# Performance work log

Hardware: AMD Instinct MI355X
Metric: run time of the kernel (lower is better)

The kernel has to match this reference:

```python
import jax, jax.numpy as jnp
import numpy as np

HIDDEN_SIZE = 2048
NUM_Q_HEADS = 16
NUM_KV_HEADS = 4
HEAD_DIM = 128
EPS = 1e-6
B, T = 1, 4096


def rms_norm(x, w):
    xf = x.astype(jnp.float32)
    n = xf * jax.lax.rsqrt(jnp.mean(xf * xf, axis=-1, keepdims=True) + EPS)
    return (n * w.astype(jnp.float32)).astype(x.dtype)


def rotate_half(x):
    x1, x2 = jnp.split(x, 2, axis=-1)
    return jnp.concatenate([-x2, x1], axis=-1)


def apply_rope(x, cos, sin):
    # x: [B, H, T, D]; cos/sin: [B, T, D]
    return x * cos[:, None, :, :] + rotate_half(x) * sin[:, None, :, :]


def setup_inputs() -> dict:
    key = jax.random.key(0)
    ks = jax.random.split(key, 6)
    s = 0.02
    x = jax.random.normal(ks[0], (B, T, HIDDEN_SIZE), dtype=jnp.float32)
    position_ids = jnp.arange(T, dtype=jnp.int64 if jax.config.jax_enable_x64 else jnp.int32)[None, :].repeat(B, axis=0)
    inv_freq = (1.0 / (10000.0 ** (np.arange(0, HEAD_DIM, 2, dtype=np.float32) / HEAD_DIM))).astype(np.float32)
    inv_freq = jnp.asarray(inv_freq)
    Wq = jax.random.normal(ks[1], (HIDDEN_SIZE, NUM_Q_HEADS * HEAD_DIM * 2), dtype=jnp.float32) * s
    Wk = jax.random.normal(ks[2], (HIDDEN_SIZE, NUM_KV_HEADS * HEAD_DIM), dtype=jnp.float32) * s
    Wv = jax.random.normal(ks[3], (HIDDEN_SIZE, NUM_KV_HEADS * HEAD_DIM), dtype=jnp.float32) * s
    Wo = jax.random.normal(ks[4], (NUM_Q_HEADS * HEAD_DIM, HIDDEN_SIZE), dtype=jnp.float32) * s
    q_norm_w = jnp.ones((HEAD_DIM,), dtype=jnp.float32)
    k_norm_w = jnp.ones((HEAD_DIM,), dtype=jnp.float32)
    return {"x": x, "position_ids": position_ids, "inv_freq": inv_freq,
            "Wq": Wq, "Wk": Wk, "Wv": Wv, "Wo": Wo,
            "q_norm_w": q_norm_w, "k_norm_w": k_norm_w}


def reference(x, position_ids, inv_freq, Wq, Wk, Wv, Wo, q_norm_w, k_norm_w):
    Bb, Tt, _ = x.shape
    dtype = x.dtype
    qg = (x @ Wq).reshape(Bb, Tt, NUM_Q_HEADS, HEAD_DIM * 2)
    q, gate = qg[..., :HEAD_DIM], qg[..., HEAD_DIM:]
    gate = gate.reshape(Bb, Tt, NUM_Q_HEADS * HEAD_DIM)
    k = (x @ Wk).reshape(Bb, Tt, NUM_KV_HEADS, HEAD_DIM)
    v = (x @ Wv).reshape(Bb, Tt, NUM_KV_HEADS, HEAD_DIM)
    q = rms_norm(q, q_norm_w)
    k = rms_norm(k, k_norm_w)
    q = q.transpose(0, 2, 1, 3)  # [B, Hq, T, D]
    k = k.transpose(0, 2, 1, 3)  # [B, Hkv, T, D]
    v = v.transpose(0, 2, 1, 3)
    # RoPE angles: [B, T, D/2] -> concat -> [B, T, D]
    freqs = position_ids.astype(jnp.float32)[:, :, None] * inv_freq[None, None, :]
    emb = jnp.concatenate([freqs, freqs], axis=-1)
    cos, sin = jnp.cos(emb).astype(dtype), jnp.sin(emb).astype(dtype)
    q = apply_rope(q, cos, sin)
    k = apply_rope(k, cos, sin)
    groups = NUM_Q_HEADS // NUM_KV_HEADS
    k = jnp.repeat(k, groups, axis=1)  # [B, Hq, T, D]
    v = jnp.repeat(v, groups, axis=1)
    scale = HEAD_DIM ** -0.5
    attn = jnp.einsum('bhqd,bhkd->bhqk', q, k) * scale
    causal = jnp.tril(jnp.ones((Tt, Tt), dtype=bool))
    attn = jnp.where(causal[None, None, :, :], attn, jnp.array(-jnp.inf, dtype=attn.dtype))
    attn = jax.nn.softmax(attn.astype(jnp.float32), axis=-1).astype(dtype)
    out = jnp.einsum('bhqk,bhkd->bhqd', attn, v)
    out = out.transpose(0, 2, 1, 3).reshape(Bb, Tt, NUM_Q_HEADS * HEAD_DIM)
    out = out * jax.nn.sigmoid(gate)
    return out @ Wo
```

## Files before the change

### kernel.cpp

```cpp
#include <hip/hip_runtime.h>
#include <hip/hip_bf16.h>

#define T_SEQ 4096
#define HID 2048
#define NQH 16
#define NKVH 4
#define HD 128
#define KVW (NKVH * HD)
#define KVSTRIDE 1024
#define QGW (NQH * HD * 2)

typedef __attribute__((ext_vector_type(8))) short short8;
typedef __attribute__((ext_vector_type(4))) float f32x4;
typedef __attribute__((ext_vector_type(16))) float f32x16;
typedef __hip_bfloat16 bf16;

__device__ inline float bf2f(bf16 v) { return __bfloat162float(v); }
__device__ inline bf16 f2bf(float v) { return __float2bfloat16(v); }

__device__ inline void storeC(float* p, float v) { *p = v; }
__device__ inline void storeC(bf16* p, float v) { *p = f2bf(v); }

__device__ inline void gload16(const void* g, void* l) {
    __builtin_amdgcn_global_load_lds(
        (const __attribute__((address_space(1))) void*)g,
        (__attribute__((address_space(3))) void*)l, 16, 0, 0);
}

__device__ inline unsigned pack2(float a, float b) {
    union { bf16 h[2]; unsigned u; } x;
    x.h[0] = f2bf(a); x.h[1] = f2bf(b);
    return x.u;
}
union U8 { unsigned u[4]; short8 s; };

__global__ void rope_tables(const int* __restrict__ pos, const float* __restrict__ inv_freq,
                            float* __restrict__ cosT, float* __restrict__ sinT) {
    int id = blockIdx.x * 256 + threadIdx.x;
    int t = id >> 6, i = id & 63;
    float f = (float)pos[t] * inv_freq[i];
    cosT[id] = cosf(f);
    sinT[id] = sinf(f);
}

__global__ void cvt_bf16(const float* __restrict__ in, bf16* __restrict__ out, int n) {
    int id = (blockIdx.x * 256 + threadIdx.x) * 4;
    if (id >= n) return;
    float4 v = *(const float4*)(in + id);
    bf16 tmp[4] = {f2bf(v.x), f2bf(v.y), f2bf(v.z), f2bf(v.w)};
    *(uint2*)(out + id) = *(uint2*)tmp;
}

__global__ void cvt_transpose(const float* __restrict__ in, bf16* __restrict__ out, int R, int C) {
    __shared__ float tile[32][33];
    int tx = threadIdx.x, ty = threadIdx.y;
    int r0 = blockIdx.y * 32, c0 = blockIdx.x * 32;
#pragma unroll
    for (int k = 0; k < 4; ++k)
        tile[ty + 8 * k][tx] = in[(long)(r0 + ty + 8 * k) * C + c0 + tx];
    __syncthreads();
#pragma unroll
    for (int k = 0; k < 4; ++k)
        out[(long)(c0 + ty + 8 * k) * R + r0 + tx] = f2bf(tile[tx][ty + 8 * k]);
}

__global__ void transpose_v(const bf16* __restrict__ kvb, bf16* __restrict__ vT) {
    __shared__ bf16 tile[32][33];
    int tx = threadIdx.x, ty = threadIdx.y;
    int d0 = blockIdx.x * 32, t0 = blockIdx.y * 32;
#pragma unroll
    for (int k = 0; k < 4; ++k)
        tile[ty + 8 * k][tx] = kvb[(long)(t0 + ty + 8 * k) * KVSTRIDE + KVW + d0 + tx];
    __syncthreads();
#pragma unroll
    for (int k = 0; k < 4; ++k)
        vT[(long)(d0 + ty + 8 * k) * T_SEQ + t0 + tx] = tile[tx][ty + 8 * k];
}

template <typename OutT>
__global__ __launch_bounds__(256) void gemm_bt(const bf16* __restrict__ A,
                                               const bf16* __restrict__ Bt,
                                               OutT* __restrict__ C, int M, int N, int K) {
    __shared__ __align__(16) bf16 As[128 * 32];
    __shared__ __align__(16) bf16 Bs[128 * 32];
    const int tid = threadIdx.x, lane = tid & 63, wv = tid >> 6;
    const int nwg = gridDim.x * gridDim.y;
    const int orig = blockIdx.y * gridDim.x + blockIdx.x;
    const int wg = (orig & 7) * (nwg >> 3) + (orig >> 3);
    const int bm = (wg / gridDim.x) * 128, bn = (wg % gridDim.x) * 128;
    const int wm = (wv >> 1) * 64, wn = (wv & 1) * 64;
    const int lr = lane & 15, lg = lane >> 4;
    f32x4 acc[4][4] = {};
    const int srow = tid >> 2, skg = (tid & 3) * 8;
    const bf16* aP = A + (long)(bm + srow) * K + skg;
    const bf16* bP = Bt + (long)(bn + srow) * K + skg;
    bf16* asBase = As + wv * 512;
    bf16* bsBase = Bs + wv * 512;
    for (int kt = 0; kt < K; kt += 32) {
        __syncthreads();
        gload16(aP + kt, asBase);
        gload16(aP + (long)64 * K + kt, asBase + 2048);
        gload16(bP + kt, bsBase);
        gload16(bP + (long)64 * K + kt, bsBase + 2048);
        __syncthreads();
        short8 af[4], bfv[4];
#pragma unroll
        for (int m = 0; m < 4; ++m)
            af[m] = *(const short8*)(As + (wm + m * 16 + lr) * 32 + lg * 8);
#pragma unroll
        for (int n = 0; n < 4; ++n)
            bfv[n] = *(const short8*)(Bs + (wn + n * 16 + lr) * 32 + lg * 8);
#pragma unroll
        for (int m = 0; m < 4; ++m)
#pragma unroll
            for (int n = 0; n < 4; ++n)
                acc[m][n] = __builtin_amdgcn_mfma_f32_16x16x32_bf16(af[m], bfv[n], acc[m][n], 0, 0, 0);
    }
#pragma unroll
    for (int m = 0; m < 4; ++m)
#pragma unroll
        for (int n = 0; n < 4; ++n)
#pragma unroll
            for (int j = 0; j < 4; ++j) {
                int r = bm + wm + m * 16 + lg * 4 + j;
                int c = bn + wn + n * 16 + lr;
                storeC(&C[(long)r * N + c], acc[m][n][j]);
            }
}

#define STAGEA256(T, hh)                                                                     \
    {                                                                                        \
        const int b_ = (T) & 1;                                                              \
        gload16(aSrc + (long)((hh) * 128) * K + (long)(T) * 64, &As[b_][(hh) * 8192 + wv * 512]); \
        gload16(aSrc + (long)((hh) * 128 + 64) * K + (long)(T) * 64,                         \
                &As[b_][(hh) * 8192 + 4096 + wv * 512]);                                     \
    }
#define STAGEB256(T, hh)                                                                     \
    {                                                                                        \
        const int b_ = (T) & 1;                                                              \
        gload16(bSrc + (long)((hh) * 128) * K + (long)(T) * 64, &Bs[b_][(hh) * 8192 + wv * 512]); \
        gload16(bSrc + (long)((hh) * 128 + 64) * K + (long)(T) * 64,                         \
                &Bs[b_][(hh) * 8192 + 4096 + wv * 512]);                                     \
    }

template <typename OutT>
__global__ __launch_bounds__(512, 2) void gemm256(const bf16* __restrict__ A,
                                                  const bf16* __restrict__ Bt,
                                                  OutT* __restrict__ C, int M, int N, int K) {
    __shared__ __align__(16) bf16 As[2][256 * 64];
    __shared__ __align__(16) bf16 Bs[2][256 * 64];
    const int tid = threadIdx.x, lane = tid & 63, wv = tid >> 6;
    const int wr = wv >> 2, wc = wv & 3;
    const int lr = lane & 15, lg = lane >> 4;
    const int bm = blockIdx.y * 256, bn = blockIdx.x * 256;
    const int nt = K >> 6;

    const int srow = tid >> 3, sslot = tid & 7;
    const int slotLog = sslot ^ (srow & 7);
    const bf16* aSrc = A + (long)(bm + srow) * K + slotLog * 8;
    const bf16* bSrc = Bt + (long)(bn + srow) * K + slotLog * 8;

    int slotE[2];
#pragma unroll
    for (int ks = 0; ks < 2; ++ks) slotE[ks] = ((ks * 4 + lg) ^ (lr & 7)) * 8;

    f32x4 acc[8][4] = {};

    STAGEB256(0, 0); STAGEB256(0, 1);
    STAGEA256(0, 0); STAGEA256(0, 1);
    STAGEB256(1, 0); STAGEB256(1, 1);
    asm volatile("s_waitcnt vmcnt(4)" ::: "memory");
    __builtin_amdgcn_s_barrier();

    for (int t = 0; t < nt; ++t) {
        const int cur = t & 1;
        const bf16* Acur = As[cur];
        const bf16* Bcur = Bs[cur];
        short8 bfr[8];
#pragma unroll
        for (int q = 0; q < 4; ++q) {
            if (q == 0) {
#pragma unroll
                for (int fn = 0; fn < 4; ++fn)
#pragma unroll
                    for (int ks = 0; ks < 2; ++ks)
                        bfr[fn * 2 + ks] =
                            *(const short8*)(Bcur + (wc * 64 + fn * 16 + lr) * 64 + slotE[ks]);
            }
            short8 afr[4];
#pragma unroll
            for (int f2 = 0; f2 < 2; ++f2)
#pragma unroll
                for (int ks = 0; ks < 2; ++ks)
                    afr[f2 * 2 + ks] =
                        *(const short8*)(Acur + (wr * 128 + (q * 2 + f2) * 16 + lr) * 64 + slotE[ks]);
            if (q == 0) { if (t + 1 < nt) STAGEA256(t + 1, 0); }
            else if (q == 1) { if (t + 1 < nt) STAGEA256(t + 1, 1); }
            else if (q == 2) { if (t + 2 < nt) STAGEB256(t + 2, 0); }
            else { if (t + 2 < nt) STAGEB256(t + 2, 1); }
            __builtin_amdgcn_s_barrier();
            __builtin_amdgcn_s_setprio(1);
#pragma unroll
            for (int f2 = 0; f2 < 2; ++f2)
#pragma unroll
                for (int fn = 0; fn < 4; ++fn)
#pragma unroll
                    for (int ks = 0; ks < 2; ++ks)
                        acc[q * 2 + f2][fn] = __builtin_amdgcn_mfma_f32_16x16x32_bf16(
                            afr[f2 * 2 + ks], bfr[fn * 2 + ks], acc[q * 2 + f2][fn], 0, 0, 0);
            __builtin_amdgcn_s_setprio(0);
            if (q == 3) asm volatile("s_waitcnt vmcnt(4)" ::: "memory");
            __builtin_amdgcn_s_barrier();
        }
    }

#pragma unroll
    for (int fm = 0; fm < 8; ++fm)
#pragma unroll
        for (int fn = 0; fn < 4; ++fn)
#pragma unroll
            for (int j = 0; j < 4; ++j) {
                int r = bm + wr * 128 + fm * 16 + lg * 4 + j;
                int c = bn + wc * 64 + fn * 16 + lr;
                storeC(&C[(long)r * N + c], acc[fm][fn][j]);
            }
}

__global__ __launch_bounds__(256) void norm_rope(bf16* __restrict__ buf, int rowStride,
                                                 int headStride, int hshift,
                                                 const float* __restrict__ w,
                                                 const float* __restrict__ cosT,
                                                 const float* __restrict__ sinT,
                                                 float outScale) {
    int row = blockIdx.x * 4 + (threadIdx.x >> 6);
    int lane = threadIdx.x & 63;
    int t = row >> hshift, h = row & ((1 << hshift) - 1);
    bf16* p = buf + (long)t * rowStride + h * headStride;
    float x1 = bf2f(p[lane]), x2 = bf2f(p[lane + 64]);
    float ss = x1 * x1 + x2 * x2;
    ss += __shfl_xor(ss, 1);
    ss += __shfl_xor(ss, 2);
    ss += __shfl_xor(ss, 4);
    ss += __shfl_xor(ss, 8);
    ss += __shfl_xor(ss, 16);
    ss += __shfl_xor(ss, 32);
    float r = rsqrtf(ss * (1.0f / 128.0f) + 1e-6f);
    float c = cosT[t * 64 + lane], s = sinT[t * 64 + lane];
    float n1 = x1 * r * w[lane], n2 = x2 * r * w[lane + 64];
    p[lane] = f2bf((n1 * c - n2 * s) * outScale);
    p[lane + 64] = f2bf((n2 * c + n1 * s) * outScale);
}

__global__ __launch_bounds__(256, 2) void attn9(const bf16* __restrict__ qg,
                                                const bf16* __restrict__ kvb,
                                                const bf16* __restrict__ vT,
                                                bf16* __restrict__ aout) {
    __shared__ __align__(16) bf16 Ks[2][64 * 128];
    __shared__ __align__(16) bf16 Vs[2][128 * 64];
    const int tid = threadIdx.x, lane = tid & 63, wv = tid >> 6;
    const int q32 = lane & 31, g = lane >> 5;
    const int bid = blockIdx.x;
    const int xcd = bid & 7, slot = bid >> 3;
    const int h = 2 * xcd + (slot & 1);
    const int chunk = 31 - (slot >> 1);
    const int hk = h >> 2;
    const int q0w = chunk * 128 + wv * 32;
    const int nkt = 2 * chunk + 2;
    const int qr = q0w + q32;

    short8 bq[8];
    {
        const bf16* qp = qg + (long)(q0w + q32) * QGW + h * (HD * 2) + g * 8;
#pragma unroll
        for (int kk = 0; kk < 8; ++kk) bq[kk] = *(const short8*)(qp + kk * 16);
    }

    f32x16 acc[4] = {};
    f32x16 accL = {};
    float m2 = -1e30f;
    const short8 vONE = {16256, 16256, 16256, 16256, 16256, 16256, 16256, 16256};

    const bf16* kS[4];
    const bf16* vS[4];
    int kOff[4], vOff[4];
#pragma unroll
    for (int i = 0; i < 4; ++i) {
        const int kc = wv * 4 + i;
        const int krow = kc * 4 + (lane >> 4);
        const int kcolB = ((lane & 15) * 16) ^ ((krow & 15) << 4);
        kS[i] = kvb + (long)krow * KVSTRIDE + hk * HD + (kcolB >> 1);
        kOff[i] = kc * 512;
        const int vc = wv * 4 + i;
        const int vrow = vc * 8 + (lane >> 3);
        const int vcolB = ((lane & 7) * 16) ^ ((vrow & 7) << 4);
        vS[i] = vT + (long)(hk * HD + vrow) * T_SEQ + (vcolB >> 1);
        vOff[i] = vc * 512;
    }

#pragma unroll
    for (int i = 0; i < 4; ++i) gload16(kS[i], &Ks[0][kOff[i]]);
#pragma unroll
    for (int i = 0; i < 4; ++i) gload16(vS[i], &Vs[0][vOff[i]]);
    __syncthreads();

    const int kSlotB = (g * 16) ^ ((q32 & 15) << 4);
    const int vSlotB = (g * 16) ^ ((q32 & 7) << 4);

    for (int kt = 0; kt < nkt; ++kt) {
        const int cur = kt & 1;
        if (kt + 1 < nkt) {
            const long koff = (long)(kt + 1) * 64;
#pragma unroll
            for (int i = 0; i < 4; ++i) gload16(kS[i] + koff * KVSTRIDE, &Ks[cur ^ 1][kOff[i]]);
#pragma unroll
            for (int i = 0; i < 4; ++i) gload16(vS[i] + koff, &Vs[cur ^ 1][vOff[i]]);
        }
        const int key00 = kt * 64;
        if (key00 <= q0w + 31) {
            const bf16* KsB = Ks[cur];
            const bf16* VsB = Vs[cur];
            f32x16 s0 = {}, s1 = {};
#pragma unroll
            for (int kk = 0; kk < 8; ++kk) {
                const int ko = q32 * 128 + (((kk * 32) ^ kSlotB) >> 1);
                short8 ka0 = *(const short8*)(KsB + ko);
                short8 ka1 = *(const short8*)(KsB + ko + 4096);
                s0 = __builtin_amdgcn_mfma_f32_32x32x16_bf16(ka0, bq[kk], s0, 0, 0, 0);
                s1 = __builtin_amdgcn_mfma_f32_32x32x16_bf16(ka1, bq[kk], s1, 0, 0, 0);
            }
            if (key00 + 63 > q0w) {
#pragma unroll
                for (int r = 0; r < 16; ++r) {
                    const int krow = (r & 3) + 8 * (r >> 2) + 4 * g;
                    if (key00 + krow > qr) s0[r] = -1e30f;
                    if (key00 + 32 + krow > qr) s1[r] = -1e30f;
                }
            }
            float t8[8];
#pragma unroll
            for (int i = 0; i < 8; ++i)
                t8[i] = fmaxf(fmaxf(s0[i], s0[i + 8]), fmaxf(s1[i], s1[i + 8]));
            float mx = fmaxf(fmaxf(fmaxf(t8[0], t8[1]), fmaxf(t8[2], t8[3])),
                             fmaxf(fmaxf(t8[4], t8[5]), fmaxf(t8[6], t8[7])));
            mx = fmaxf(mx, __shfl_xor(mx, 32));
            float mn = m2, e = 1.f;
            bool need = false;
            if (mx > m2 + 8.f) { mn = mx; e = exp2f(m2 - mx); need = true; }
            m2 = mn;
#pragma unroll
            for (int r = 0; r < 16; ++r) {
                s0[r] = exp2f(s0[r] - mn);
                s1[r] = exp2f(s1[r] - mn);
            }
            if (__any(need)) {
#pragma unroll
                for (int r = 0; r < 16; ++r) {
                    const int krow = (r & 3) + 8 * (r >> 2) + 4 * g;
                    float er = __shfl(e, krow);
#pragma unroll
                    for (int n = 0; n < 4; ++n) acc[n][r] *= er;
                    accL[r] *= er;
                }
            }
            short8 pa[4];
#pragma unroll
            for (int half = 0; half < 2; ++half) {
                const f32x16& p = half ? s1 : s0;
                unsigned lo0 = pack2(p[0], p[1]),   lo1 = pack2(p[2], p[3]);
                unsigned hi0 = pack2(p[4], p[5]),   hi1 = pack2(p[6], p[7]);
                unsigned lo2 = pack2(p[8], p[9]),   lo3 = pack2(p[10], p[11]);
                unsigned hi2 = pack2(p[12], p[13]), hi3 = pack2(p[14], p[15]);
                unsigned sw0 = __shfl_xor(g ? lo0 : hi0, 32);
                unsigned sw1 = __shfl_xor(g ? lo1 : hi1, 32);
                unsigned sw2 = __shfl_xor(g ? lo2 : hi2, 32);
                unsigned sw3 = __shfl_xor(g ? lo3 : hi3, 32);
                U8 a0, a1;
                a0.u[0] = g ? sw0 : lo0;  a0.u[1] = g ? sw1 : lo1;
                a0.u[2] = g ? hi0 : sw0;  a0.u[3] = g ? hi1 : sw1;
                a1.u[0] = g ? sw2 : lo2;  a1.u[1] = g ? sw3 : lo3;
                a1.u[2] = g ? hi2 : sw2;  a1.u[3] = g ? hi3 : sw3;
                pa[half * 2] = a0.s;
                pa[half * 2 + 1] = a1.s;
            }
#pragma unroll
            for (int ks = 0; ks < 4; ++ks) {
                const int vo = q32 * 64 + (((ks * 32) ^ vSlotB) >> 1);
#pragma unroll
                for (int n = 0; n < 4; ++n) {
                    short8 vb = *(const short8*)(VsB + vo + n * 2048);
                    acc[n] = __builtin_amdgcn_mfma_f32_32x32x16_bf16(pa[ks], vb, acc[n], 0, 0, 0);
                }
                accL = __builtin_amdgcn_mfma_f32_32x32x16_bf16(pa[ks], vONE, accL, 0, 0, 0);
            }
        }
        __syncthreads();
    }

#pragma unroll
    for (int r = 0; r < 16; ++r) {
        const int krow = (r & 3) + 8 * (r >> 2) + 4 * g;
        const float linv = 1.0f / accL[r];
        const long t = q0w + krow;
        const bf16* gp = qg + t * QGW + h * (HD * 2) + HD + q32;
        bf16* op = aout + t * (NQH * HD) + h * HD + q32;
#pragma unroll
        for (int n = 0; n < 4; ++n) {
            float gv = bf2f(gp[n * 32]);
            float o = acc[n][r] * linv * (1.f / (1.f + __expf(-gv)));
            op[n * 32] = f2bf(o);
        }
    }
}

extern "C" void kernel_launch(void* const* d_in, const int* in_sizes, int n_in,
                              void* d_out, int out_size, void* d_ws, size_t ws_size,
                              hipStream_t stream) {
    const float* x = (const float*)d_in[0];
    const int* pos = (const int*)d_in[1];
    const float* inv_freq = (const float*)d_in[2];
    const float* Wq = (const float*)d_in[3];
    const float* Wk = (const float*)d_in[4];
    const float* Wv = (const float*)d_in[5];
    const float* Wo = (const float*)d_in[6];
    const float* qw = (const float*)d_in[7];
    const float* kw = (const float*)d_in[8];
    float* out = (float*)d_out;

    char* ws = (char*)d_ws;
    float* cosT = (float*)ws;               ws += (long)T_SEQ * 64 * 4;
    float* sinT = (float*)ws;               ws += (long)T_SEQ * 64 * 4;
    bf16* bx = (bf16*)ws;                   ws += (long)T_SEQ * HID * 2;
    bf16* bWq = (bf16*)ws;                  ws += (long)QGW * HID * 2;
    bf16* bKV = (bf16*)ws;                  ws += (long)KVSTRIDE * HID * 2;
    bf16* bWo = (bf16*)ws;                  ws += (long)HID * HID * 2;
    bf16* qg = (bf16*)ws;                   ws += (long)T_SEQ * QGW * 2;
    bf16* kvb = (bf16*)ws;                  ws += (long)T_SEQ * KVSTRIDE * 2;
    bf16* aout = (bf16*)ws;                 ws += (long)T_SEQ * (NQH * HD) * 2;
    bf16* vT = (bf16*)bWq;

    rope_tables<<<T_SEQ * 64 / 256, 256, 0, stream>>>(pos, inv_freq, cosT, sinT);
    cvt_bf16<<<(T_SEQ * HID / 4 + 255) / 256, 256, 0, stream>>>(x, bx, T_SEQ * HID);
    cvt_transpose<<<dim3(QGW / 32, HID / 32), dim3(32, 8), 0, stream>>>(Wq, bWq, HID, QGW);
    cvt_transpose<<<dim3(KVW / 32, HID / 32), dim3(32, 8), 0, stream>>>(Wk, bKV, HID, KVW);
    cvt_transpose<<<dim3(KVW / 32, HID / 32), dim3(32, 8), 0, stream>>>(Wv, bKV + (long)KVW * HID, HID, KVW);
    cvt_transpose<<<dim3(HID / 32, HID / 32), dim3(32, 8), 0, stream>>>(Wo, bWo, HID, HID);

    gemm256<bf16><<<dim3(QGW / 256, T_SEQ / 256), 512, 0, stream>>>(bx, bWq, qg, T_SEQ, QGW, HID);
    gemm_bt<bf16><<<dim3(KVSTRIDE / 128, T_SEQ / 128), 256, 0, stream>>>(bx, bKV, kvb, T_SEQ, KVSTRIDE, HID);

    transpose_v<<<dim3(KVW / 32, T_SEQ / 32), dim3(32, 8), 0, stream>>>(kvb, vT);
    norm_rope<<<(T_SEQ * NQH) / 4, 256, 0, stream>>>(qg, QGW, HD * 2, 4, qw, cosT, sinT,
                                                     0.08838834764831845f * 1.4426950408889634f);
    norm_rope<<<(T_SEQ * NKVH) / 4, 256, 0, stream>>>(kvb, KVSTRIDE, HD, 2, kw, cosT, sinT, 1.0f);

    attn9<<<dim3(512), 256, 0, stream>>>(qg, kvb, vT, aout);

    gemm256<float><<<dim3(HID / 256, T_SEQ / 256), 512, 0, stream>>>(aout, bWo, out, T_SEQ, HID, NQH * HD);
}
```

Measured before the change: 364.6 us.

## Single-buffer K tile in attention for higher occupancy; narrow output GEMM tile

The attention kernel drops the double-buffered K tile in shared memory, adds a barrier after QK^T, and then prefetches the next K tile, raising launch bounds to 3 blocks per CU. The output projection GEMM becomes templated on tile width and uses BN=128, which doubles the block count (256 instead of 128) to fill more CUs. The cost is an extra sync per key tile and less K prefetch overlap in attention, plus lower per-block reuse in the GEMM.

```diff
diff --git a/kernel.cpp b/kernel.cpp
--- a/kernel.cpp
+++ b/kernel.cpp
@@ -128,31 +128,17 @@
             }
 }
 
-#define STAGEA256(T, hh)                                                                     \
-    {                                                                                        \
-        const int b_ = (T) & 1;                                                              \
-        gload16(aSrc + (long)((hh) * 128) * K + (long)(T) * 64, &As[b_][(hh) * 8192 + wv * 512]); \
-        gload16(aSrc + (long)((hh) * 128 + 64) * K + (long)(T) * 64,                         \
-                &As[b_][(hh) * 8192 + 4096 + wv * 512]);                                     \
-    }
-#define STAGEB256(T, hh)                                                                     \
-    {                                                                                        \
-        const int b_ = (T) & 1;                                                              \
-        gload16(bSrc + (long)((hh) * 128) * K + (long)(T) * 64, &Bs[b_][(hh) * 8192 + wv * 512]); \
-        gload16(bSrc + (long)((hh) * 128 + 64) * K + (long)(T) * 64,                         \
-                &Bs[b_][(hh) * 8192 + 4096 + wv * 512]);                                     \
-    }
-
-template <typename OutT>
+template <int BN, typename OutT>
 __global__ __launch_bounds__(512, 2) void gemm256(const bf16* __restrict__ A,
                                                   const bf16* __restrict__ Bt,
                                                   OutT* __restrict__ C, int M, int N, int K) {
+    constexpr int FN = BN / 64;
     __shared__ __align__(16) bf16 As[2][256 * 64];
-    __shared__ __align__(16) bf16 Bs[2][256 * 64];
+    __shared__ __align__(16) bf16 Bs[2][BN * 64];
     const int tid = threadIdx.x, lane = tid & 63, wv = tid >> 6;
     const int wr = wv >> 2, wc = wv & 3;
     const int lr = lane & 15, lg = lane >> 4;
-    const int bm = blockIdx.y * 256, bn = blockIdx.x * 256;
+    const int bm = blockIdx.y * 256, bn = blockIdx.x * BN;
     const int nt = K >> 6;
 
     const int srow = tid >> 3, sslot = tid & 7;
@@ -160,32 +146,46 @@
     const bf16* aSrc = A + (long)(bm + srow) * K + slotLog * 8;
     const bf16* bSrc = Bt + (long)(bn + srow) * K + slotLog * 8;
 
+    auto stageA = [&](int T, int hh) {
+        const int b_ = T & 1;
+        gload16(aSrc + (long)(hh * 128) * K + (long)T * 64, &As[b_][hh * 8192 + wv * 512]);
+        gload16(aSrc + (long)(hh * 128 + 64) * K + (long)T * 64, &As[b_][hh * 8192 + 4096 + wv * 512]);
+    };
+    auto stageB = [&](int T, int hh) {
+        const int b_ = T & 1;
+        gload16(bSrc + (long)(hh * 128) * K + (long)T * 64, &Bs[b_][hh * 8192 + wv * 512]);
+        gload16(bSrc + (long)(hh * 128 + 64) * K + (long)T * 64, &Bs[b_][hh * 8192 + 4096 + wv * 512]);
+    };
+
     int slotE[2];
 #pragma unroll
     for (int ks = 0; ks < 2; ++ks) slotE[ks] = ((ks * 4 + lg) ^ (lr & 7)) * 8;
 
-    f32x4 acc[8][4] = {};
-
-    STAGEB256(0, 0); STAGEB256(0, 1);
-    STAGEA256(0, 0); STAGEA256(0, 1);
-    STAGEB256(1, 0); STAGEB256(1, 1);
-    asm volatile("s_waitcnt vmcnt(4)" ::: "memory");
+    f32x4 acc[8][FN] = {};
+
+    stageB(0, 0);
+    if constexpr (BN == 256) stageB(0, 1);
+    stageA(0, 0); stageA(0, 1);
+    stageB(1, 0);
+    if constexpr (BN == 256) stageB(1, 1);
+    if constexpr (BN == 256) asm volatile("s_waitcnt vmcnt(4)" ::: "memory");
+    else                     asm volatile("s_waitcnt vmcnt(2)" ::: "memory");
     __builtin_amdgcn_s_barrier();
 
     for (int t = 0; t < nt; ++t) {
         const int cur = t & 1;
         const bf16* Acur = As[cur];
         const bf16* Bcur = Bs[cur];
-        short8 bfr[8];
+        short8 bfr[FN * 2];
 #pragma unroll
         for (int q = 0; q < 4; ++q) {
             if (q == 0) {
 #pragma unroll
-                for (int fn = 0; fn < 4; ++fn)
+                for (int fn = 0; fn < FN; ++fn)
 #pragma unroll
                     for (int ks = 0; ks < 2; ++ks)
                         bfr[fn * 2 + ks] =
-                            *(const short8*)(Bcur + (wc * 64 + fn * 16 + lr) * 64 + slotE[ks]);
+                            *(const short8*)(Bcur + (wc * (BN / 4) + fn * 16 + lr) * 64 + slotE[ks]);
             }
             short8 afr[4];
 #pragma unroll
@@ -194,22 +194,25 @@
                 for (int ks = 0; ks < 2; ++ks)
                     afr[f2 * 2 + ks] =
                         *(const short8*)(Acur + (wr * 128 + (q * 2 + f2) * 16 + lr) * 64 + slotE[ks]);
-            if (q == 0) { if (t + 1 < nt) STAGEA256(t + 1, 0); }
-            else if (q == 1) { if (t + 1 < nt) STAGEA256(t + 1, 1); }
-            else if (q == 2) { if (t + 2 < nt) STAGEB256(t + 2, 0); }
-            else { if (t + 2 < nt) STAGEB256(t + 2, 1); }
+            if (q == 0) { if (t + 1 < nt) stageA(t + 1, 0); }
+            else if (q == 1) { if (t + 1 < nt) stageA(t + 1, 1); }
+            else if (q == 2) { if (t + 2 < nt) stageB(t + 2, 0); }
+            else { if (BN == 256 && t + 2 < nt) stageB(t + 2, 1); }
             __builtin_amdgcn_s_barrier();
             __builtin_amdgcn_s_setprio(1);
 #pragma unroll
             for (int f2 = 0; f2 < 2; ++f2)
 #pragma unroll
-                for (int fn = 0; fn < 4; ++fn)
+                for (int fn = 0; fn < FN; ++fn)
 #pragma unroll
                     for (int ks = 0; ks < 2; ++ks)
                         acc[q * 2 + f2][fn] = __builtin_amdgcn_mfma_f32_16x16x32_bf16(
                             afr[f2 * 2 + ks], bfr[fn * 2 + ks], acc[q * 2 + f2][fn], 0, 0, 0);
             __builtin_amdgcn_s_setprio(0);
-            if (q == 3) asm volatile("s_waitcnt vmcnt(4)" ::: "memory");
+            if (q == 3) {
+                if constexpr (BN == 256) asm volatile("s_waitcnt vmcnt(4)" ::: "memory");
+                else                     asm volatile("s_waitcnt vmcnt(2)" ::: "memory");
+            }
             __builtin_amdgcn_s_barrier();
         }
     }
@@ -217,11 +220,11 @@
 #pragma unroll
     for (int fm = 0; fm < 8; ++fm)
 #pragma unroll
-        for (int fn = 0; fn < 4; ++fn)
+        for (int fn = 0; fn < FN; ++fn)
 #pragma unroll
             for (int j = 0; j < 4; ++j) {
                 int r = bm + wr * 128 + fm * 16 + lg * 4 + j;
-                int c = bn + wc * 64 + fn * 16 + lr;
+                int c = bn + wc * (BN / 4) + fn * 16 + lr;
                 storeC(&C[(long)r * N + c], acc[fm][fn][j]);
             }
 }
@@ -251,11 +254,11 @@
     p[lane + 64] = f2bf((n2 * c + n1 * s) * outScale);
 }
 
-__global__ __launch_bounds__(256, 2) void attn9(const bf16* __restrict__ qg,
-                                                const bf16* __restrict__ kvb,
-                                                const bf16* __restrict__ vT,
-                                                bf16* __restrict__ aout) {
-    __shared__ __align__(16) bf16 Ks[2][64 * 128];
+__global__ __launch_bounds__(256, 3) void attn10(const bf16* __restrict__ qg,
+                                                 const bf16* __restrict__ kvb,
+                                                 const bf16* __restrict__ vT,
+                                                 bf16* __restrict__ aout) {
+    __shared__ __align__(16) bf16 Ks[64 * 128];
     __shared__ __align__(16) bf16 Vs[2][128 * 64];
     const int tid = threadIdx.x, lane = tid & 63, wv = tid >> 6;
     const int q32 = lane & 31, g = lane >> 5;
@@ -298,7 +301,7 @@
     }
 
 #pragma unroll
-    for (int i = 0; i < 4; ++i) gload16(kS[i], &Ks[0][kOff[i]]);
+    for (int i = 0; i < 4; ++i) gload16(kS[i], &Ks[kOff[i]]);
 #pragma unroll
     for (int i = 0; i < 4; ++i) gload16(vS[i], &Vs[0][vOff[i]]);
     __syncthreads();
@@ -308,26 +311,31 @@
 
     for (int kt = 0; kt < nkt; ++kt) {
         const int cur = kt & 1;
+        const int key00 = kt * 64;
+        const bool compute = (key00 <= q0w + 31);
         if (kt + 1 < nkt) {
             const long koff = (long)(kt + 1) * 64;
 #pragma unroll
-            for (int i = 0; i < 4; ++i) gload16(kS[i] + koff * KVSTRIDE, &Ks[cur ^ 1][kOff[i]]);
-#pragma unroll
             for (int i = 0; i < 4; ++i) gload16(vS[i] + koff, &Vs[cur ^ 1][vOff[i]]);
         }
-        const int key00 = kt * 64;
-        if (key00 <= q0w + 31) {
-            const bf16* KsB = Ks[cur];
-            const bf16* VsB = Vs[cur];
-            f32x16 s0 = {}, s1 = {};
+        f32x16 s0 = {}, s1 = {};
+        if (compute) {
 #pragma unroll
             for (int kk = 0; kk < 8; ++kk) {
                 const int ko = q32 * 128 + (((kk * 32) ^ kSlotB) >> 1);
-                short8 ka0 = *(const short8*)(KsB + ko);
-                short8 ka1 = *(const short8*)(KsB + ko + 4096);
+                short8 ka0 = *(const short8*)(Ks + ko);
+                short8 ka1 = *(const short8*)(Ks + ko + 4096);
                 s0 = __builtin_amdgcn_mfma_f32_32x32x16_bf16(ka0, bq[kk], s0, 0, 0, 0);
                 s1 = __builtin_amdgcn_mfma_f32_32x32x16_bf16(ka1, bq[kk], s1, 0, 0, 0);
             }
+        }
+        __syncthreads();
+        if (kt + 1 < nkt) {
+            const long koff = (long)(kt + 1) * 64;
+#pragma unroll
+            for (int i = 0; i < 4; ++i) gload16(kS[i] + koff * KVSTRIDE, &Ks[kOff[i]]);
+        }
+        if (compute) {
             if (key00 + 63 > q0w) {
 #pragma unroll
                 for (int r = 0; r < 16; ++r) {
@@ -382,6 +390,7 @@
                 pa[half * 2] = a0.s;
                 pa[half * 2 + 1] = a1.s;
             }
+            const bf16* VsB = Vs[cur];
 #pragma unroll
             for (int ks = 0; ks < 4; ++ks) {
                 const int vo = q32 * 64 + (((ks * 32) ^ vSlotB) >> 1);
@@ -445,7 +454,7 @@
     cvt_transpose<<<dim3(KVW / 32, HID / 32), dim3(32, 8), 0, stream>>>(Wv, bKV + (long)KVW * HID, HID, KVW);
     cvt_transpose<<<dim3(HID / 32, HID / 32), dim3(32, 8), 0, stream>>>(Wo, bWo, HID, HID);
 
-    gemm256<bf16><<<dim3(QGW / 256, T_SEQ / 256), 512, 0, stream>>>(bx, bWq, qg, T_SEQ, QGW, HID);
+    gemm256<256, bf16><<<dim3(QGW / 256, T_SEQ / 256), 512, 0, stream>>>(bx, bWq, qg, T_SEQ, QGW, HID);
     gemm_bt<bf16><<<dim3(KVSTRIDE / 128, T_SEQ / 128), 256, 0, stream>>>(bx, bKV, kvb, T_SEQ, KVSTRIDE, HID);
 
     transpose_v<<<dim3(KVW / 32, T_SEQ / 32), dim3(32, 8), 0, stream>>>(kvb, vT);
@@ -453,7 +462,7 @@
                                                      0.08838834764831845f * 1.4426950408889634f);
     norm_rope<<<(T_SEQ * NKVH) / 4, 256, 0, stream>>>(kvb, KVSTRIDE, HD, 2, kw, cosT, sinT, 1.0f);
 
-    attn9<<<dim3(512), 256, 0, stream>>>(qg, kvb, vT, aout);
-
-    gemm256<float><<<dim3(HID / 256, T_SEQ / 256), 512, 0, stream>>>(aout, bWo, out, T_SEQ, HID, NQH * HD);
-}
+    attn10<<<dim3(512), 256, 0, stream>>>(qg, kvb, vT, aout);
+
+    gemm256<128, float><<<dim3(HID / 128, T_SEQ / 256), 512, 0, stream>>>(aout, bWo, out, T_SEQ, HID, NQH * HD);
+}
```

After: 523.4 us. +43.6%, slower.
